# Kernel optimization log

Hardware: AMD Instinct MI355X
Metric: run time of the kernel (lower is better)

The kernel has to match this reference:

```python
import jax, jax.numpy as jnp
import numpy as np
import math

B, N, T, F_IN, F_OUT = 32, 512, 12, 64, 64


def setup_inputs() -> dict:
    key = jax.random.key(0)
    k1, k2, k3 = jax.random.split(key, 3)
    x = jax.random.normal(k1, (B, N, T, F_IN), dtype=jnp.float32)
    adj = jax.random.uniform(k2, (N, N), dtype=jnp.float32)  # sym_norm_Adj_matrix
    W_theta = jax.random.normal(k3, (F_OUT, F_IN), dtype=jnp.float32) * (1.0 / math.sqrt(F_IN))
    return {"x": x, "adj": adj, "W_theta": W_theta}


def reference(x, adj, W_theta):
    # x: (B, N, T, F)
    b, n, t, f = x.shape
    scale = 1.0 / math.sqrt(f)
    # (B, T, N, F)
    xt = jnp.transpose(x, (0, 2, 1, 3))
    # attention scores per (batch, time): QK^T / sqrt(F), softmax over last dim,
    # then an extra 1/sqrt(F) scaling as in the original forward
    score = jnp.einsum('btnf,btmf->btnm', xt, xt) * scale
    att = jax.nn.softmax(score, axis=-1) * scale  # dropout p=0
    # post-softmax multiplicative adjacency mask, then aggregate neighbor features
    agg = jnp.einsum('btnm,btmf->btnf', adj[None, None] * att, xt)
    # Theta linear (no bias) + ReLU, back to (B, N, T, F_out)
    out = jax.nn.relu(jnp.einsum('btnf,of->btno', agg, W_theta))
    return jnp.transpose(out, (0, 2, 1, 3))
```

## Files before the change

kernel.cpp:

```cpp
#include <hip/hip_runtime.h>
#include <math.h>

#define NN 512
#define TT 12
#define FF 64

typedef float  f32x4   __attribute__((ext_vector_type(4)));
typedef float  f32x16  __attribute__((ext_vector_type(16)));
typedef short  short4v __attribute__((ext_vector_type(4)));
typedef short  short8v __attribute__((ext_vector_type(8)));
typedef _Float16 h16x4 __attribute__((ext_vector_type(4)));
typedef _Float16 h16x8 __attribute__((ext_vector_type(8)));
typedef unsigned int u32;
typedef u32    u32x4   __attribute__((ext_vector_type(4)));

static __device__ __forceinline__ u32 pkrtz(float a, float b) {
    u32 p;
    asm("v_cvt_pkrtz_f16_f32 %0, %1, %2" : "=v"(p) : "v"(a), "v"(b));
    return p;
}
static __device__ __forceinline__ void cvt4h(f32x4 v, short4v& h, short4v& lo) {
    h16x4 hh, ll;
    #pragma unroll
    for (int j = 0; j < 4; ++j) {
        _Float16 a = (_Float16)v[j];
        hh[j] = a;
        ll[j] = (_Float16)(v[j] - (float)a);
    }
    h  = __builtin_bit_cast(short4v, hh);
    lo = __builtin_bit_cast(short4v, ll);
}
static __device__ __forceinline__ short8v cat44(short4v a, short4v b) {
    return __builtin_shufflevector(a, b, 0, 1, 2, 3, 4, 5, 6, 7);
}
static __device__ __forceinline__ f32x16 mfmah(short8v a, short8v b, f32x16 c) {
    return __builtin_amdgcn_mfma_f32_32x32x16_f16(
        __builtin_bit_cast(h16x8, a), __builtin_bit_cast(h16x8, b), c, 0, 0, 0);
}

#define BUFSZ 26112
#define SMEM_BYTES 52736

__global__ __launch_bounds__(256, 3)
void sgcn12(const float* __restrict__ x, const float* __restrict__ adj,
            const float* __restrict__ W, float* __restrict__ out)
{
    __shared__ __align__(16) char smem[SMEM_BYTES];
    char* sA = smem;
    float* linvLDS = (float*)(smem + 2 * BUFSZ);

    const int d   = blockIdx.x;
    const int xcd = d & 7;
    const int s   = d >> 3;
    const int G   = xcd + 8 * (s >> 2);
    const int mem = s & 3;
    const int t = G % TT, b = G / TT;
    const int n0 = mem * 128;

    const int tid = threadIdx.x;
    const int w   = tid >> 6;
    const int l31 = tid & 31;
    const int hi2 = (tid >> 5) & 1;
    const int fq  = tid & 15;
    const int mq  = tid >> 4;
    const int myn = n0 + 32 * w + l31;

    const float K2 = 0.18033688011112042f;
    const float SH2 = 8.656170245333781f;

    const float* xnrow = x + ((size_t)(b * NN + myn) * TT + t) * FF;
    short8v xnH[4];
    #pragma unroll
    for (int ks = 0; ks < 4; ++ks) {
        f32x4 a0 = *(const f32x4*)(xnrow + ks * 16 + hi2 * 8);
        f32x4 a1 = *(const f32x4*)(xnrow + ks * 16 + hi2 * 8 + 4);
        short4v h0, l0, h1, l1;
        cvt4h(a0, h0, l0);
        cvt4h(a1, h1, l1);
        xnH[ks] = cat44(h0, h1);
    }

    short4v sh[4], sq[4];

#define STAGE_CONVERT(L0, L1, L2, L3)                                          \
    { cvt4h(L0, sh[0], sq[0]); cvt4h(L1, sh[1], sq[1]);                        \
      cvt4h(L2, sh[2], sq[2]); cvt4h(L3, sh[3], sq[3]); }

#define STAGE_LDS_WRITE(DST)                                                   \
  {                                                                            \
    char* dKH = (DST);                                                         \
    char* dKL = (DST) + 8704;                                                  \
    char* dKT = (DST) + 17408;                                                 \
    _Pragma("unroll")                                                          \
    for (int j = 0; j < 4; ++j) {                                              \
        *(short4v*)(dKH + ((4*mq+j)*68 + 4*fq) * 2) = sh[j];                   \
        *(short4v*)(dKL + ((4*mq+j)*68 + 4*fq) * 2) = sq[j];                   \
    }                                                                          \
    _Pragma("unroll")                                                          \
    for (int j = 0; j < 4; ++j) {                                              \
        short4v th; th[0]=sh[0][j]; th[1]=sh[1][j]; th[2]=sh[2][j]; th[3]=sh[3][j]; \
        *(short4v*)(dKT + ((4*fq+j)*68 + 4*mq) * 2) = th;                      \
    }                                                                          \
  }

    {
        const float* xst = x + ((size_t)(b * NN + 4 * mq) * TT + t) * FF + 4 * fq;
        f32x4 ld0 = *(const f32x4*)(xst);
        f32x4 ld1 = *(const f32x4*)(xst + TT * FF);
        f32x4 ld2 = *(const f32x4*)(xst + 2 * TT * FF);
        f32x4 ld3 = *(const f32x4*)(xst + 3 * TT * FF);
        STAGE_CONVERT(ld0, ld1, ld2, ld3)
        STAGE_LDS_WRITE(smem)
    }
    __syncthreads();

    float lp4[4] = {0.f, 0.f, 0.f, 0.f};
    f32x16 agg0a, agg0b, agg1a, agg1b;
    #pragma unroll
    for (int i = 0; i < 16; ++i) { agg0a[i]=0.f; agg0b[i]=0.f; agg1a[i]=0.f; agg1b[i]=0.f; }

    unsigned bo = 0;
    for (int mt = 0; mt < 8; ++mt) {
        const int m0 = mt * 64;
        const char* bKH = smem + bo;
        const char* bKL = smem + bo + 8704;
        const char* bKT = smem + bo + 17408;

        f32x4 p0, p1, p2, p3;
        if (mt < 7) {
            const float* xs = x + ((size_t)(b * NN + m0 + 64 + 4 * mq) * TT + t) * FF + 4 * fq;
            p0 = *(const f32x4*)(xs);
            p1 = *(const f32x4*)(xs + TT * FF);
            p2 = *(const f32x4*)(xs + 2 * TT * FF);
            p3 = *(const f32x4*)(xs + 3 * TT * FF);
        }

        const float* arow0 = adj + (size_t)myn * NN + m0 + 4 * hi2;
        f32x4 a00 = *(const f32x4*)(arow0);
        f32x4 a01 = *(const f32x4*)(arow0 + 8);
        f32x4 a02 = *(const f32x4*)(arow0 + 16);
        f32x4 a03 = *(const f32x4*)(arow0 + 24);

        short8v pa[4];

        f32x16 scA, scB;
        #pragma unroll
        for (int i = 0; i < 16; ++i) { scA[i] = 0.f; scB[i] = 0.f; }
        #pragma unroll
        for (int ks = 0; ks < 2; ++ks) {
            short4v k0 = *(const short4v*)(bKH + (l31 * 68 + ks*16 + hi2*8) * 2);
            short4v k1 = *(const short4v*)(bKH + (l31 * 68 + ks*16 + hi2*8 + 4) * 2);
            short4v q0 = *(const short4v*)(bKL + (l31 * 68 + ks*16 + hi2*8) * 2);
            short4v q1 = *(const short4v*)(bKL + (l31 * 68 + ks*16 + hi2*8 + 4) * 2);
            scA = mfmah(cat44(k0, k1), xnH[ks], scA);
            scA = mfmah(cat44(q0, q1), xnH[ks], scA);
        }
        #pragma unroll
        for (int ks = 2; ks < 4; ++ks) {
            short4v k0 = *(const short4v*)(bKH + (l31 * 68 + ks*16 + hi2*8) * 2);
            short4v k1 = *(const short4v*)(bKH + (l31 * 68 + ks*16 + hi2*8 + 4) * 2);
            short4v q0 = *(const short4v*)(bKL + (l31 * 68 + ks*16 + hi2*8) * 2);
            short4v q1 = *(const short4v*)(bKL + (l31 * 68 + ks*16 + hi2*8 + 4) * 2);
            scB = mfmah(cat44(k0, k1), xnH[ks], scB);
            scB = mfmah(cat44(q0, q1), xnH[ks], scB);
        }

        const float* arow1 = adj + (size_t)myn * NN + m0 + 32 + 4 * hi2;
        f32x4 a10 = *(const f32x4*)(arow1);
        f32x4 a11 = *(const f32x4*)(arow1 + 8);
        f32x4 a12 = *(const f32x4*)(arow1 + 16);
        f32x4 a13 = *(const f32x4*)(arow1 + 24);

        {
            f32x16 sc = scA + scB;
            float p[16];
            #pragma unroll
            for (int r = 0; r < 16; ++r) {
                p[r] = __builtin_amdgcn_exp2f(sc[r] * K2 - SH2);
                lp4[r & 3] += p[r];
            }
            p[0] *= a00[0]; p[1] *= a00[1]; p[2]  *= a00[2]; p[3]  *= a00[3];
            p[4] *= a01[0]; p[5] *= a01[1]; p[6]  *= a01[2]; p[7]  *= a01[3];
            p[8] *= a02[0]; p[9] *= a02[1]; p[10] *= a02[2]; p[11] *= a02[3];
            p[12]*= a03[0]; p[13]*= a03[1]; p[14] *= a03[2]; p[15] *= a03[3];
            u32 A0 = pkrtz(p[0],  p[1]),  A1 = pkrtz(p[2],  p[3]);
            u32 B0 = pkrtz(p[4],  p[5]),  B1 = pkrtz(p[6],  p[7]);
            u32 A2 = pkrtz(p[8],  p[9]),  A3 = pkrtz(p[10], p[11]);
            u32 B2 = pkrtz(p[12], p[13]), B3 = pkrtz(p[14], p[15]);
            u32 sA0 = (u32)__shfl_xor((int)A0, 32), sA1 = (u32)__shfl_xor((int)A1, 32);
            u32 sB0 = (u32)__shfl_xor((int)B0, 32), sB1 = (u32)__shfl_xor((int)B1, 32);
            u32 sA2 = (u32)__shfl_xor((int)A2, 32), sA3 = (u32)__shfl_xor((int)A3, 32);
            u32 sB2 = (u32)__shfl_xor((int)B2, 32), sB3 = (u32)__shfl_xor((int)B3, 32);
            u32x4 e, o;
            e[0] = hi2 ? sB0 : A0;  e[1] = hi2 ? sB1 : A1;
            e[2] = hi2 ? B0 : sA0;  e[3] = hi2 ? B1 : sA1;
            o[0] = hi2 ? sB2 : A2;  o[1] = hi2 ? sB3 : A3;
            o[2] = hi2 ? B2 : sA2;  o[3] = hi2 ? B3 : sA3;
            pa[0] = __builtin_bit_cast(short8v, e);
            pa[1] = __builtin_bit_cast(short8v, o);
        }

        {
            short4v v0 = *(const short4v*)(bKT + (l31 * 68 + hi2*8) * 2);
            short4v v1 = *(const short4v*)(bKT + (l31 * 68 + hi2*8 + 4) * 2);
            agg0a = mfmah(pa[0], cat44(v0, v1), agg0a);
            short4v w0 = *(const short4v*)(bKT + ((32 + l31) * 68 + hi2*8) * 2);
            short4v w1 = *(const short4v*)(bKT + ((32 + l31) * 68 + hi2*8 + 4) * 2);
            agg1a = mfmah(pa[0], cat44(w0, w1), agg1a);
            short4v v2 = *(const short4v*)(bKT + (l31 * 68 + 16 + hi2*8) * 2);
            short4v v3 = *(const short4v*)(bKT + (l31 * 68 + 16 + hi2*8 + 4) * 2);
            agg0b = mfmah(pa[1], cat44(v2, v3), agg0b);
            short4v w2 = *(const short4v*)(bKT + ((32 + l31) * 68 + 16 + hi2*8) * 2);
            short4v w3 = *(const short4v*)(bKT + ((32 + l31) * 68 + 16 + hi2*8 + 4) * 2);
            agg1b = mfmah(pa[1], cat44(w2, w3), agg1b);
        }

        #pragma unroll
        for (int i = 0; i < 16; ++i) { scA[i] = 0.f; scB[i] = 0.f; }
        #pragma unroll
        for (int ks = 0; ks < 2; ++ks) {
            short4v k0 = *(const short4v*)(bKH + ((32 + l31) * 68 + ks*16 + hi2*8) * 2);
            short4v k1 = *(const short4v*)(bKH + ((32 + l31) * 68 + ks*16 + hi2*8 + 4) * 2);
            short4v q0 = *(const short4v*)(bKL + ((32 + l31) * 68 + ks*16 + hi2*8) * 2);
            short4v q1 = *(const short4v*)(bKL + ((32 + l31) * 68 + ks*16 + hi2*8 + 4) * 2);
            scA = mfmah(cat44(k0, k1), xnH[ks], scA);
            scA = mfmah(cat44(q0, q1), xnH[ks], scA);
        }
        #pragma unroll
        for (int ks = 2; ks < 4; ++ks) {
            short4v k0 = *(const short4v*)(bKH + ((32 + l31) * 68 + ks*16 + hi2*8) * 2);
            short4v k1 = *(const short4v*)(bKH + ((32 + l31) * 68 + ks*16 + hi2*8 + 4) * 2);
            short4v q0 = *(const short4v*)(bKL + ((32 + l31) * 68 + ks*16 + hi2*8) * 2);
            short4v q1 = *(const short4v*)(bKL + ((32 + l31) * 68 + ks*16 + hi2*8 + 4) * 2);
            scB = mfmah(cat44(k0, k1), xnH[ks], scB);
            scB = mfmah(cat44(q0, q1), xnH[ks], scB);
        }

        {
            f32x16 sc = scA + scB;
            float p[16];
            #pragma unroll
            for (int r = 0; r < 16; ++r) {
                p[r] = __builtin_amdgcn_exp2f(sc[r] * K2 - SH2);
                lp4[r & 3] += p[r];
            }
            p[0] *= a10[0]; p[1] *= a10[1]; p[2]  *= a10[2]; p[3]  *= a10[3];
            p[4] *= a11[0]; p[5] *= a11[1]; p[6]  *= a11[2]; p[7]  *= a11[3];
            p[8] *= a12[0]; p[9] *= a12[1]; p[10] *= a12[2]; p[11] *= a12[3];
            p[12]*= a13[0]; p[13]*= a13[1]; p[14] *= a13[2]; p[15] *= a13[3];
            u32 A0 = pkrtz(p[0],  p[1]),  A1 = pkrtz(p[2],  p[3]);
            u32 B0 = pkrtz(p[4],  p[5]),  B1 = pkrtz(p[6],  p[7]);
            u32 A2 = pkrtz(p[8],  p[9]),  A3 = pkrtz(p[10], p[11]);
            u32 B2 = pkrtz(p[12], p[13]), B3 = pkrtz(p[14], p[15]);
            u32 sA0 = (u32)__shfl_xor((int)A0, 32), sA1 = (u32)__shfl_xor((int)A1, 32);
            u32 sB0 = (u32)__shfl_xor((int)B0, 32), sB1 = (u32)__shfl_xor((int)B1, 32);
            u32 sA2 = (u32)__shfl_xor((int)A2, 32), sA3 = (u32)__shfl_xor((int)A3, 32);
            u32 sB2 = (u32)__shfl_xor((int)B2, 32), sB3 = (u32)__shfl_xor((int)B3, 32);
            u32x4 e, o;
            e[0] = hi2 ? sB0 : A0;  e[1] = hi2 ? sB1 : A1;
            e[2] = hi2 ? B0 : sA0;  e[3] = hi2 ? B1 : sA1;
            o[0] = hi2 ? sB2 : A2;  o[1] = hi2 ? sB3 : A3;
            o[2] = hi2 ? B2 : sA2;  o[3] = hi2 ? B3 : sA3;
            pa[2] = __builtin_bit_cast(short8v, e);
            pa[3] = __builtin_bit_cast(short8v, o);
        }

        {
            short4v v0 = *(const short4v*)(bKT + (l31 * 68 + 32 + hi2*8) * 2);
            short4v v1 = *(const short4v*)(bKT + (l31 * 68 + 32 + hi2*8 + 4) * 2);
            agg0a = mfmah(pa[2], cat44(v0, v1), agg0a);
            short4v w0 = *(const short4v*)(bKT + ((32 + l31) * 68 + 32 + hi2*8) * 2);
            short4v w1 = *(const short4v*)(bKT + ((32 + l31) * 68 + 32 + hi2*8 + 4) * 2);
            agg1a = mfmah(pa[2], cat44(w0, w1), agg1a);
            short4v v2 = *(const short4v*)(bKT + (l31 * 68 + 48 + hi2*8) * 2);
            short4v v3 = *(const short4v*)(bKT + (l31 * 68 + 48 + hi2*8 + 4) * 2);
            agg0b = mfmah(pa[3], cat44(v2, v3), agg0b);
            short4v w2 = *(const short4v*)(bKT + ((32 + l31) * 68 + 48 + hi2*8) * 2);
            short4v w3 = *(const short4v*)(bKT + ((32 + l31) * 68 + 48 + hi2*8 + 4) * 2);
            agg1b = mfmah(pa[3], cat44(w2, w3), agg1b);
        }

        if (mt < 7) {
            STAGE_CONVERT(p0, p1, p2, p3)
            STAGE_LDS_WRITE(smem + (bo ^ BUFSZ))
        }
        __syncthreads();
        bo ^= BUFSZ;
    }

    f32x16 agg0 = agg0a + agg0b;
    f32x16 agg1 = agg1a + agg1b;
    float lpart = (lp4[0] + lp4[1]) + (lp4[2] + lp4[3]);
    float lf = lpart + __shfl_xor(lpart, 32);
    if (hi2 == 0) linvLDS[32 * w + l31] = 0.125f / lf;
    __syncthreads();

    #pragma unroll
    for (int r = 0; r < 16; ++r) {
        int row = 32 * w + (r & 3) + 8 * (r >> 2) + 4 * hi2;
        float nv = linvLDS[row];
        _Float16 h0 = (_Float16)(agg0[r] * nv);
        _Float16 h1 = (_Float16)(agg1[r] * nv);
        *(short*)(sA + (row * 68 + l31) * 2)      = __builtin_bit_cast(short, h0);
        *(short*)(sA + (row * 68 + 32 + l31) * 2) = __builtin_bit_cast(short, h1);
    }
    __syncthreads();

    short8v gH[4];
    #pragma unroll
    for (int ks = 0; ks < 4; ++ks) {
        short4v a0 = *(const short4v*)(sA + ((32*w + l31) * 68 + ks*16 + hi2*8) * 2);
        short4v a1 = *(const short4v*)(sA + ((32*w + l31) * 68 + ks*16 + hi2*8 + 4) * 2);
        gH[ks] = cat44(a0, a1);
    }

    #pragma unroll
    for (int ob = 0; ob < 2; ++ob) {
        short8v wHreg[4], wLreg[4];
        #pragma unroll
        for (int ks = 0; ks < 4; ++ks) {
            const float* wp = W + (size_t)(ob * 32 + l31) * FF + ks * 16 + hi2 * 8;
            f32x4 wa = *(const f32x4*)(wp);
            f32x4 wb = *(const f32x4*)(wp + 4);
            short4v h0, l0, h1, l1;
            cvt4h(wa, h0, l0);
            cvt4h(wb, h1, l1);
            wHreg[ks] = cat44(h0, h1);
            wLreg[ks] = cat44(l0, l1);
        }
        f32x16 oc;
        #pragma unroll
        for (int i = 0; i < 16; ++i) oc[i] = 0.f;
        #pragma unroll
        for (int ks = 0; ks < 4; ++ks) {
            oc = mfmah(gH[ks], wHreg[ks], oc);
            oc = mfmah(gH[ks], wLreg[ks], oc);
        }
        #pragma unroll
        for (int r = 0; r < 16; ++r) {
            int row = 32 * w + (r & 3) + 8 * (r >> 2) + 4 * hi2;
            out[((size_t)(b * NN + n0 + row) * TT + t) * FF + 32 * ob + l31] = fmaxf(oc[r], 0.f);
        }
    }
#undef STAGE_CONVERT
#undef STAGE_LDS_WRITE
}

extern "C" void kernel_launch(void* const* d_in, const int* in_sizes, int n_in,
                              void* d_out, int out_size, void* d_ws, size_t ws_size,
                              hipStream_t stream) {
    const float* x   = (const float*)d_in[0];
    const float* adj = (const float*)d_in[1];
    const float* W   = (const float*)d_in[2];
    float* outp = (float*)d_out;

    sgcn12<<<dim3(1536), dim3(256), 0, stream>>>(x, adj, W, outp);
}
```

Baseline: 90.90 us.

## Move fp16 hi/lo split from staged keys to register-resident queries, shrink LDS

The kernel now keeps the high and low fp16 halves of the block's own query rows in registers and stages only the high fp16 half of each key tile in LDS. Dropping the low-part key buffer shrinks each LDS stage and lowers total LDS so four blocks per CU can fit instead of three, with launch bounds raised to match. The split score and aggregate accumulators are merged into single chains, cutting registers but serialising the MFMA dependencies. Error compensation now applies to the query side instead of the key side, which changes rounding slightly.

```diff
diff --git a/kernel.cpp b/kernel.cpp
--- a/kernel.cpp
+++ b/kernel.cpp
@@ -30,6 +30,12 @@
     h  = __builtin_bit_cast(short4v, hh);
     lo = __builtin_bit_cast(short4v, ll);
 }
+static __device__ __forceinline__ short4v cvt4hi(f32x4 v) {
+    h16x4 hh;
+    #pragma unroll
+    for (int j = 0; j < 4; ++j) hh[j] = (_Float16)v[j];
+    return __builtin_bit_cast(short4v, hh);
+}
 static __device__ __forceinline__ short8v cat44(short4v a, short4v b) {
     return __builtin_shufflevector(a, b, 0, 1, 2, 3, 4, 5, 6, 7);
 }
@@ -38,11 +44,11 @@
         __builtin_bit_cast(h16x8, a), __builtin_bit_cast(h16x8, b), c, 0, 0, 0);
 }
 
-#define BUFSZ 26112
-#define SMEM_BYTES 52736
-
-__global__ __launch_bounds__(256, 3)
-void sgcn12(const float* __restrict__ x, const float* __restrict__ adj,
+#define BUFSZ 17408
+#define SMEM_BYTES 35328
+
+__global__ __launch_bounds__(256, 4)
+void sgcn14(const float* __restrict__ x, const float* __restrict__ adj,
             const float* __restrict__ W, float* __restrict__ out)
 {
     __shared__ __align__(16) char smem[SMEM_BYTES];
@@ -69,7 +75,7 @@
     const float SH2 = 8.656170245333781f;
 
     const float* xnrow = x + ((size_t)(b * NN + myn) * TT + t) * FF;
-    short8v xnH[4];
+    short8v xnH[4], xnL[4];
     #pragma unroll
     for (int ks = 0; ks < 4; ++ks) {
         f32x4 a0 = *(const f32x4*)(xnrow + ks * 16 + hi2 * 8);
@@ -78,24 +84,22 @@
         cvt4h(a0, h0, l0);
         cvt4h(a1, h1, l1);
         xnH[ks] = cat44(h0, h1);
-    }
-
-    short4v sh[4], sq[4];
+        xnL[ks] = cat44(l0, l1);
+    }
+
+    short4v sh[4];
 
 #define STAGE_CONVERT(L0, L1, L2, L3)                                          \
-    { cvt4h(L0, sh[0], sq[0]); cvt4h(L1, sh[1], sq[1]);                        \
-      cvt4h(L2, sh[2], sq[2]); cvt4h(L3, sh[3], sq[3]); }
+    { sh[0] = cvt4hi(L0); sh[1] = cvt4hi(L1);                                  \
+      sh[2] = cvt4hi(L2); sh[3] = cvt4hi(L3); }
 
 #define STAGE_LDS_WRITE(DST)                                                   \
   {                                                                            \
     char* dKH = (DST);                                                         \
-    char* dKL = (DST) + 8704;                                                  \
-    char* dKT = (DST) + 17408;                                                 \
+    char* dKT = (DST) + 8704;                                                  \
     _Pragma("unroll")                                                          \
-    for (int j = 0; j < 4; ++j) {                                              \
+    for (int j = 0; j < 4; ++j)                                                \
         *(short4v*)(dKH + ((4*mq+j)*68 + 4*fq) * 2) = sh[j];                   \
-        *(short4v*)(dKL + ((4*mq+j)*68 + 4*fq) * 2) = sq[j];                   \
-    }                                                                          \
     _Pragma("unroll")                                                          \
     for (int j = 0; j < 4; ++j) {                                              \
         short4v th; th[0]=sh[0][j]; th[1]=sh[1][j]; th[2]=sh[2][j]; th[3]=sh[3][j]; \
@@ -115,16 +119,15 @@
     __syncthreads();
 
     float lp4[4] = {0.f, 0.f, 0.f, 0.f};
-    f32x16 agg0a, agg0b, agg1a, agg1b;
-    #pragma unroll
-    for (int i = 0; i < 16; ++i) { agg0a[i]=0.f; agg0b[i]=0.f; agg1a[i]=0.f; agg1b[i]=0.f; }
+    f32x16 agg0, agg1;
+    #pragma unroll
+    for (int i = 0; i < 16; ++i) { agg0[i] = 0.f; agg1[i] = 0.f; }
 
     unsigned bo = 0;
     for (int mt = 0; mt < 8; ++mt) {
         const int m0 = mt * 64;
         const char* bKH = smem + bo;
-        const char* bKL = smem + bo + 8704;
-        const char* bKT = smem + bo + 17408;
+        const char* bKT = smem + bo + 8704;
 
         f32x4 p0, p1, p2, p3;
         if (mt < 7) {
@@ -143,36 +146,19 @@
 
         short8v pa[4];
 
-        f32x16 scA, scB;
-        #pragma unroll
-        for (int i = 0; i < 16; ++i) { scA[i] = 0.f; scB[i] = 0.f; }
-        #pragma unroll
-        for (int ks = 0; ks < 2; ++ks) {
+        f32x16 sc;
+        #pragma unroll
+        for (int i = 0; i < 16; ++i) sc[i] = 0.f;
+        #pragma unroll
+        for (int ks = 0; ks < 4; ++ks) {
             short4v k0 = *(const short4v*)(bKH + (l31 * 68 + ks*16 + hi2*8) * 2);
             short4v k1 = *(const short4v*)(bKH + (l31 * 68 + ks*16 + hi2*8 + 4) * 2);
-            short4v q0 = *(const short4v*)(bKL + (l31 * 68 + ks*16 + hi2*8) * 2);
-            short4v q1 = *(const short4v*)(bKL + (l31 * 68 + ks*16 + hi2*8 + 4) * 2);
-            scA = mfmah(cat44(k0, k1), xnH[ks], scA);
-            scA = mfmah(cat44(q0, q1), xnH[ks], scA);
-        }
-        #pragma unroll
-        for (int ks = 2; ks < 4; ++ks) {
-            short4v k0 = *(const short4v*)(bKH + (l31 * 68 + ks*16 + hi2*8) * 2);
-            short4v k1 = *(const short4v*)(bKH + (l31 * 68 + ks*16 + hi2*8 + 4) * 2);
-            short4v q0 = *(const short4v*)(bKL + (l31 * 68 + ks*16 + hi2*8) * 2);
-            short4v q1 = *(const short4v*)(bKL + (l31 * 68 + ks*16 + hi2*8 + 4) * 2);
-            scB = mfmah(cat44(k0, k1), xnH[ks], scB);
-            scB = mfmah(cat44(q0, q1), xnH[ks], scB);
-        }
-
-        const float* arow1 = adj + (size_t)myn * NN + m0 + 32 + 4 * hi2;
-        f32x4 a10 = *(const f32x4*)(arow1);
-        f32x4 a11 = *(const f32x4*)(arow1 + 8);
-        f32x4 a12 = *(const f32x4*)(arow1 + 16);
-        f32x4 a13 = *(const f32x4*)(arow1 + 24);
+            short8v kk = cat44(k0, k1);
+            sc = mfmah(kk, xnH[ks], sc);
+            sc = mfmah(kk, xnL[ks], sc);
+        }
 
         {
-            f32x16 sc = scA + scB;
             float p[16];
             #pragma unroll
             for (int r = 0; r < 16; ++r) {
@@ -200,44 +186,39 @@
             pa[1] = __builtin_bit_cast(short8v, o);
         }
 
+        const float* arow1 = adj + (size_t)myn * NN + m0 + 32 + 4 * hi2;
+        f32x4 a10 = *(const f32x4*)(arow1);
+        f32x4 a11 = *(const f32x4*)(arow1 + 8);
+        f32x4 a12 = *(const f32x4*)(arow1 + 16);
+        f32x4 a13 = *(const f32x4*)(arow1 + 24);
+
         {
             short4v v0 = *(const short4v*)(bKT + (l31 * 68 + hi2*8) * 2);
             short4v v1 = *(const short4v*)(bKT + (l31 * 68 + hi2*8 + 4) * 2);
-            agg0a = mfmah(pa[0], cat44(v0, v1), agg0a);
+            agg0 = mfmah(pa[0], cat44(v0, v1), agg0);
             short4v w0 = *(const short4v*)(bKT + ((32 + l31) * 68 + hi2*8) * 2);
             short4v w1 = *(const short4v*)(bKT + ((32 + l31) * 68 + hi2*8 + 4) * 2);
-            agg1a = mfmah(pa[0], cat44(w0, w1), agg1a);
+            agg1 = mfmah(pa[0], cat44(w0, w1), agg1);
             short4v v2 = *(const short4v*)(bKT + (l31 * 68 + 16 + hi2*8) * 2);
             short4v v3 = *(const short4v*)(bKT + (l31 * 68 + 16 + hi2*8 + 4) * 2);
-            agg0b = mfmah(pa[1], cat44(v2, v3), agg0b);
+            agg0 = mfmah(pa[1], cat44(v2, v3), agg0);
             short4v w2 = *(const short4v*)(bKT + ((32 + l31) * 68 + 16 + hi2*8) * 2);
             short4v w3 = *(const short4v*)(bKT + ((32 + l31) * 68 + 16 + hi2*8 + 4) * 2);
-            agg1b = mfmah(pa[1], cat44(w2, w3), agg1b);
-        }
-
-        #pragma unroll
-        for (int i = 0; i < 16; ++i) { scA[i] = 0.f; scB[i] = 0.f; }
-        #pragma unroll
-        for (int ks = 0; ks < 2; ++ks) {
+            agg1 = mfmah(pa[1], cat44(w2, w3), agg1);
+        }
+
+        #pragma unroll
+        for (int i = 0; i < 16; ++i) sc[i] = 0.f;
+        #pragma unroll
+        for (int ks = 0; ks < 4; ++ks) {
             short4v k0 = *(const short4v*)(bKH + ((32 + l31) * 68 + ks*16 + hi2*8) * 2);
             short4v k1 = *(const short4v*)(bKH + ((32 + l31) * 68 + ks*16 + hi2*8 + 4) * 2);
-            short4v q0 = *(const short4v*)(bKL + ((32 + l31) * 68 + ks*16 + hi2*8) * 2);
-            short4v q1 = *(const short4v*)(bKL + ((32 + l31) * 68 + ks*16 + hi2*8 + 4) * 2);
-            scA = mfmah(cat44(k0, k1), xnH[ks], scA);
-            scA = mfmah(cat44(q0, q1), xnH[ks], scA);
-        }
-        #pragma unroll
-        for (int ks = 2; ks < 4; ++ks) {
-            short4v k0 = *(const short4v*)(bKH + ((32 + l31) * 68 + ks*16 + hi2*8) * 2);
-            short4v k1 = *(const short4v*)(bKH + ((32 + l31) * 68 + ks*16 + hi2*8 + 4) * 2);
-            short4v q0 = *(const short4v*)(bKL + ((32 + l31) * 68 + ks*16 + hi2*8) * 2);
-            short4v q1 = *(const short4v*)(bKL + ((32 + l31) * 68 + ks*16 + hi2*8 + 4) * 2);
-            scB = mfmah(cat44(k0, k1), xnH[ks], scB);
-            scB = mfmah(cat44(q0, q1), xnH[ks], scB);
+            short8v kk = cat44(k0, k1);
+            sc = mfmah(kk, xnH[ks], sc);
+            sc = mfmah(kk, xnL[ks], sc);
         }
 
         {
-            f32x16 sc = scA + scB;
             float p[16];
             #pragma unroll
             for (int r = 0; r < 16; ++r) {
@@ -268,16 +249,16 @@
         {
             short4v v0 = *(const short4v*)(bKT + (l31 * 68 + 32 + hi2*8) * 2);
             short4v v1 = *(const short4v*)(bKT + (l31 * 68 + 32 + hi2*8 + 4) * 2);
-            agg0a = mfmah(pa[2], cat44(v0, v1), agg0a);
+            agg0 = mfmah(pa[2], cat44(v0, v1), agg0);
             short4v w0 = *(const short4v*)(bKT + ((32 + l31) * 68 + 32 + hi2*8) * 2);
             short4v w1 = *(const short4v*)(bKT + ((32 + l31) * 68 + 32 + hi2*8 + 4) * 2);
-            agg1a = mfmah(pa[2], cat44(w0, w1), agg1a);
+            agg1 = mfmah(pa[2], cat44(w0, w1), agg1);
             short4v v2 = *(const short4v*)(bKT + (l31 * 68 + 48 + hi2*8) * 2);
             short4v v3 = *(const short4v*)(bKT + (l31 * 68 + 48 + hi2*8 + 4) * 2);
-            agg0b = mfmah(pa[3], cat44(v2, v3), agg0b);
+            agg0 = mfmah(pa[3], cat44(v2, v3), agg0);
             short4v w2 = *(const short4v*)(bKT + ((32 + l31) * 68 + 48 + hi2*8) * 2);
             short4v w3 = *(const short4v*)(bKT + ((32 + l31) * 68 + 48 + hi2*8 + 4) * 2);
-            agg1b = mfmah(pa[3], cat44(w2, w3), agg1b);
+            agg1 = mfmah(pa[3], cat44(w2, w3), agg1);
         }
 
         if (mt < 7) {
@@ -288,8 +269,6 @@
         bo ^= BUFSZ;
     }
 
-    f32x16 agg0 = agg0a + agg0b;
-    f32x16 agg1 = agg1a + agg1b;
     float lpart = (lp4[0] + lp4[1]) + (lp4[2] + lp4[3]);
     float lf = lpart + __shfl_xor(lpart, 32);
     if (hi2 == 0) linvLDS[32 * w + l31] = 0.125f / lf;
@@ -354,5 +333,5 @@
     const float* W   = (const float*)d_in[2];
     float* outp = (float*)d_out;
 
-    sgcn12<<<dim3(1536), dim3(256), 0, stream>>>(x, adj, W, outp);
-}
+    sgcn14<<<dim3(1536), dim3(256), 0, stream>>>(x, adj, W, outp);
+}
```

After: 141.2 us. +55.3%, slower.
